# Kernel optimization log

Measured on AMD Instinct MI355X. Metric: run time of the kernel, lower is better.

## Reference

```python
import jax, jax.numpy as jnp
import numpy as np

N = 20000        # nodes (atoms)
E = 256000       # edges
H = 128          # hidden_channels == num_filters
NG = 150         # num_gaussians
L = 3            # num_interactions
B = 16           # graphs in batch
VOCAB = 256      # embed_size
CUTOFF = 15.0
LOG2 = 0.6931471805599453


def _ssp(x):
    # ShiftedSoftplus
    return jax.nn.softplus(x) - LOG2


def setup_inputs() -> dict:
    key = jax.random.key(0)
    ks = jax.random.split(key, 20)

    def w(k, shape, fan_in):
        return jax.random.normal(k, shape, jnp.float32) / np.float32(np.sqrt(fan_in))

    return {
        "z": jax.random.randint(ks[0], (N,), 0, VOCAB),
        "pos": jax.random.normal(ks[1], (N, 3), jnp.float32) * 5.0,
        "batch": jnp.sort(jax.random.randint(ks[2], (N,), 0, B)),
        "edge_index": jax.random.randint(ks[3], (2, E), 0, N),
        # parameters (weights stored as [in, out]; y = x @ W + b)
        "emb": w(ks[4], (VOCAB, H), H),
        "eu0_fc1_w": w(ks[5], (NG + 2 * H, 2 * H), NG + 2 * H),  # EdgeUpdate block 0
        "eu_fc1_w": w(ks[6], (L - 1, 3 * H, 2 * H), 3 * H),      # EdgeUpdate blocks 1..L-1
        "eu_fc1_b": jnp.zeros((L, 2 * H), jnp.float32),
        "eu_fc2_w": w(ks[7], (L, 2 * H, H), 2 * H),
        "eu_fc2_b": jnp.zeros((L, H), jnp.float32),
        "flt_w1": w(ks[8], (L, H, H), H),  # filter_mlp linear 1
        "flt_b1": jnp.zeros((L, H), jnp.float32),
        "flt_w2": w(ks[9], (L, H, H), H),  # filter_mlp linear 2
        "flt_b2": jnp.zeros((L, H), jnp.float32),
        "cf_w": w(ks[10], (L, H, H), H),   # CFConv.fc1 (no bias)
        "st_w1": w(ks[11], (L, H, H), H),  # StateMLP fc1 (no bias)
        "st_w2": w(ks[12], (L, H, H), H),  # StateMLP fc2 (no bias)
        "out_fc1_w": w(ks[13], (H, H // 2), H),
        "out_fc1_b": jnp.zeros((H // 2,), jnp.float32),
        "out_fc2_w": w(ks[14], (H // 2, 1), H // 2),
        "out_fc2_b": jnp.zeros((1,), jnp.float32),
    }


def reference(z, pos, batch, edge_index, emb, eu0_fc1_w, eu_fc1_w, eu_fc1_b,
              eu_fc2_w, eu_fc2_b, flt_w1, flt_b1, flt_w2, flt_b2, cf_w,
              st_w1, st_w2, out_fc1_w, out_fc1_b, out_fc2_w, out_fc2_b):
    row, col = edge_index[0], edge_index[1]  # source j -> target i

    h = emb[z]  # [N, H]

    # Gaussian smearing of interatomic distances
    d = jnp.linalg.norm(pos[row] - pos[col], axis=-1)  # [E]
    stop = CUTOFF - CUTOFF / NG
    offset = jnp.linspace(0.0, stop, NG, dtype=jnp.float32)
    coeff = -0.5 / (stop / (NG - 1)) ** 2
    e = jnp.exp(coeff * (d[:, None] - offset[None, :]) ** 2)  # [E, NG]

    for i in range(L):
        # EdgeUpdate: gather x_i/x_j, concat, 2-layer MLP
        cat = jnp.concatenate([h[col], h[row], e], axis=1)
        w1 = eu0_fc1_w if i == 0 else eu_fc1_w[i - 1]
        e = _ssp(cat @ w1 + eu_fc1_b[i]) @ eu_fc2_w[i] + eu_fc2_b[i]  # [E, H]

        # InteractionBlock: CFConv (filter MLP on edges, gather, modulate, scatter-add)
        W = _ssp(_ssp(e @ flt_w1[i] + flt_b1[i]) @ flt_w2[i] + flt_b2[i])  # [E, H]
        msg = (h[row] @ cf_w[i]) * W                                        # [E, H]
        m = jax.ops.segment_sum(msg, col, num_segments=N)                   # [N, H]
        # StateMLP + residual
        h = h + _ssp(m @ st_w1[i]) @ st_w2[i]

    # readout head
    h = _ssp(h @ out_fc1_w + out_fc1_b) @ out_fc2_w + out_fc2_b  # [N, 1]
    out = jax.ops.segment_sum(h, batch, num_segments=B)          # [B, 1] (readout='add')
    return out
```

## Files before the change

kernel.cpp:

```cpp
#include <hip/hip_runtime.h>
#include <hip/hip_bf16.h>
#include <math.h>

#define NN 20000
#define EE 256000
#define HH 128
#define NGAUSS 150

typedef __attribute__((ext_vector_type(8))) short bf16x8;
typedef __attribute__((ext_vector_type(4))) float f32x4;

__device__ __forceinline__ short f2bf(float f) {
  unsigned u = __builtin_bit_cast(unsigned, f);
  u += 0x7FFFu + ((u >> 16) & 1u);
  return (short)(u >> 16);
}
__device__ __forceinline__ float bf2f(short s) {
  unsigned u = ((unsigned)(unsigned short)s) << 16;
  return __builtin_bit_cast(float, u);
}
__device__ __forceinline__ float sspf(float x) {
  float t = __expf(-fabsf(x));
  return fmaxf(x, 0.f) + __logf(1.f + t) - 0.69314718055994531f;
}

struct PackDesc { const float* src; short* dst; int Kreal; int KT; int NT; int end; };
struct PackArgs { PackDesc d[24]; };

__global__ void packall_kernel(PackArgs a, int total) {
  int idx = blockIdx.x * 256 + threadIdx.x;
  if (idx >= total) return;
  int i = 0, start = 0;
  while (idx >= a.d[i].end) { start = a.d[i].end; ++i; }
  int local = idx - start;
  const float* src = a.d[i].src;
  short* dst = a.d[i].dst;
  int Kreal = a.d[i].Kreal, KT = a.d[i].KT, NT = a.d[i].NT;
  (void)KT;
  int j = local & 7;
  int lane = (local >> 3) & 63;
  int tile = local >> 9;
  int nt = tile % NT, kt = tile / NT;
  int k = kt * 32 + (lane >> 4) * 8 + j;
  int n = nt * 16 + (lane & 15);
  float w = (k < Kreal) ? src[(size_t)k * (NT * 16) + n] : 0.f;
  dst[local] = f2bf(w);
}

template <int KT, int NTW, int JSTEP = 1>
__device__ __forceinline__ void gemm_tile(const short* __restrict__ A, int as,
                                          const short* __restrict__ pack, int ktBase,
                                          int NT, int lane, int wave,
                                          f32x4 (&acc)[NTW][4]) {
  constexpr int WSTEP = (JSTEP == 1) ? NTW : 1;
  const int arow = lane & 15, agrp = lane >> 4;
  const short* abase = A + arow * as + agrp * 8;
  const short* bbase = pack + (size_t)ktBase * NT * 512 + (size_t)lane * 8;
  const int nt0 = wave * WSTEP;
  bf16x8 af[4], bh[NTW];
#pragma unroll
  for (int rg = 0; rg < 4; ++rg) af[rg] = *(const bf16x8*)(abase + rg * 16 * as);
#pragma unroll
  for (int j = 0; j < NTW; ++j)
    bh[j] = *(const bf16x8*)(bbase + (size_t)(nt0 + j * JSTEP) * 512);
#pragma unroll
  for (int kt = 0; kt < KT; ++kt) {
    bf16x8 naf[4], nbh[NTW];
    if (kt + 1 < KT) {
#pragma unroll
      for (int rg = 0; rg < 4; ++rg)
        naf[rg] = *(const bf16x8*)(abase + rg * 16 * as + (kt + 1) * 32);
#pragma unroll
      for (int j = 0; j < NTW; ++j)
        nbh[j] = *(const bf16x8*)(bbase + (size_t)((kt + 1) * NT + nt0 + j * JSTEP) * 512);
    }
#pragma unroll
    for (int j = 0; j < NTW; ++j)
#pragma unroll
      for (int rg = 0; rg < 4; ++rg)
        acc[j][rg] = __builtin_amdgcn_mfma_f32_16x16x32_bf16(af[rg], bh[j], acc[j][rg], 0, 0, 0);
    if (kt + 1 < KT) {
#pragma unroll
      for (int rg = 0; rg < 4; ++rg) af[rg] = naf[rg];
#pragma unroll
      for (int j = 0; j < NTW; ++j) bh[j] = nbh[j];
    }
  }
}

__device__ __forceinline__ void cvt16(const float4* __restrict__ src, short* dst) {
#pragma unroll
  for (int v = 0; v < 2; ++v) {
    float4 f0 = src[2 * v], f1 = src[2 * v + 1];
    union { short s[8]; uint4 u; } tm;
    tm.s[0] = f2bf(f0.x); tm.s[1] = f2bf(f0.y); tm.s[2] = f2bf(f0.z); tm.s[3] = f2bf(f0.w);
    tm.s[4] = f2bf(f1.x); tm.s[5] = f2bf(f1.y); tm.s[6] = f2bf(f1.z); tm.s[7] = f2bf(f1.w);
    *(uint4*)(dst + v * 8) = tm.u;
  }
}

__global__ __launch_bounds__(512, 4) void embedgemm_kernel(
    const int* __restrict__ z, const float* __restrict__ emb,
    const short* __restrict__ pk, short* __restrict__ h, short* __restrict__ hcf) {
  __shared__ short A[64 * 136];
  const int t = threadIdx.x, wave = t >> 6, lane = t & 63;
  const int arow = lane & 15, agrp = lane >> 4;
  const int n0 = blockIdx.x * 64;
  {
    int el = t >> 3, q = t & 7;
    int n = n0 + el;
    short* dst = A + el * 136 + q * 16;
    if (n < NN) {
      const float4* src = (const float4*)(emb + (size_t)z[n] * HH + q * 16);
      union { short s[16]; uint4 u[2]; } tm;
#pragma unroll
      for (int v = 0; v < 2; ++v) {
        float4 f0 = src[2 * v], f1 = src[2 * v + 1];
        tm.s[v * 8 + 0] = f2bf(f0.x); tm.s[v * 8 + 1] = f2bf(f0.y);
        tm.s[v * 8 + 2] = f2bf(f0.z); tm.s[v * 8 + 3] = f2bf(f0.w);
        tm.s[v * 8 + 4] = f2bf(f1.x); tm.s[v * 8 + 5] = f2bf(f1.y);
        tm.s[v * 8 + 6] = f2bf(f1.z); tm.s[v * 8 + 7] = f2bf(f1.w);
      }
      *(uint4*)dst = tm.u[0]; *(uint4*)(dst + 8) = tm.u[1];
      uint4* hg = (uint4*)(h + (size_t)n * HH + q * 16);
      hg[0] = tm.u[0]; hg[1] = tm.u[1];
    } else {
      uint4 zz = {0u, 0u, 0u, 0u};
      *(uint4*)dst = zz; *(uint4*)(dst + 8) = zz;
    }
  }
  __syncthreads();
  f32x4 zv = {0.f, 0.f, 0.f, 0.f};
  f32x4 acc[1][4];
#pragma unroll
  for (int rg = 0; rg < 4; ++rg) acc[0][rg] = zv;
  gemm_tile<4, 1>(A, 136, pk, 0, 8, lane, wave, acc);
  int col = wave * 16 + arow;
#pragma unroll
  for (int rg = 0; rg < 4; ++rg)
#pragma unroll
    for (int r = 0; r < 4; ++r) {
      int n = n0 + rg * 16 + agrp * 4 + r;
      if (n < NN) hcf[(size_t)n * HH + col] = f2bf(acc[0][rg][r]);
    }
}

template <bool FUSE>
__global__ __launch_bounds__(512, 4) void state_kernel(
    short* __restrict__ h, float* __restrict__ m,
    const short* __restrict__ p1, const short* __restrict__ p2,
    const short* __restrict__ pcf, short* __restrict__ hcf) {
  __shared__ short A[64 * 136];
  __shared__ short T[64 * 136];
  const int t = threadIdx.x, wave = t >> 6, lane = t & 63;
  const int arow = lane & 15, agrp = lane >> 4;
  const int n0 = blockIdx.x * 64;
  {
    int el = t >> 3, q = t & 7;
    int n = n0 + el;
    short* dst = A + el * 136 + q * 16;
    if (n < NN) {
      float* msrc = m + (size_t)n * HH + q * 16;
      cvt16((const float4*)msrc, dst);
      if (FUSE) {
        float4 z4 = {0.f, 0.f, 0.f, 0.f};
        float4* mz = (float4*)msrc;
        mz[0] = z4; mz[1] = z4; mz[2] = z4; mz[3] = z4;
      }
    } else {
      uint4 zz = {0u, 0u, 0u, 0u};
      *(uint4*)dst = zz; *(uint4*)(dst + 8) = zz;
    }
  }
  __syncthreads();
  f32x4 zv = {0.f, 0.f, 0.f, 0.f};
  f32x4 acc[1][4];
#pragma unroll
  for (int rg = 0; rg < 4; ++rg) acc[0][rg] = zv;
  gemm_tile<4, 1>(A, 136, p1, 0, 8, lane, wave, acc);
  int col = wave * 16 + arow;
#pragma unroll
  for (int rg = 0; rg < 4; ++rg)
#pragma unroll
    for (int r = 0; r < 4; ++r) {
      int rowl = rg * 16 + agrp * 4 + r;
      T[rowl * 136 + col] = f2bf(sspf(acc[0][rg][r]));
    }
  __syncthreads();
  short hold[16];
#pragma unroll
  for (int rg = 0; rg < 4; ++rg)
#pragma unroll
    for (int r = 0; r < 4; ++r) {
      int n = n0 + rg * 16 + agrp * 4 + r;
      hold[rg * 4 + r] = (n < NN) ? h[(size_t)n * HH + col] : (short)0;
    }
  f32x4 acc2[1][4];
#pragma unroll
  for (int rg = 0; rg < 4; ++rg) acc2[0][rg] = zv;
  gemm_tile<4, 1>(T, 136, p2, 0, 8, lane, wave, acc2);
#pragma unroll
  for (int rg = 0; rg < 4; ++rg)
#pragma unroll
    for (int r = 0; r < 4; ++r) {
      int rowl = rg * 16 + agrp * 4 + r;
      int n = n0 + rowl;
      short nb = f2bf(bf2f(hold[rg * 4 + r]) + acc2[0][rg][r]);
      if (n < NN) h[(size_t)n * HH + col] = nb;
      if (FUSE) A[rowl * 136 + col] = (n < NN) ? nb : (short)0;
    }
  if (FUSE) {
    __syncthreads();
    f32x4 acc3[1][4];
#pragma unroll
    for (int rg = 0; rg < 4; ++rg) acc3[0][rg] = zv;
    gemm_tile<4, 1>(A, 136, pcf, 0, 8, lane, wave, acc3);
#pragma unroll
    for (int rg = 0; rg < 4; ++rg)
#pragma unroll
      for (int r = 0; r < 4; ++r) {
        int n = n0 + rg * 16 + agrp * 4 + r;
        if (n < NN) hcf[(size_t)n * HH + col] = f2bf(acc3[0][rg][r]);
      }
  }
}

template <bool L0, bool WRITE_E>
__global__ __launch_bounds__(512, 4) void edge_kernel(
    const short* __restrict__ h, const short* __restrict__ hcf,
    const int* __restrict__ ei, const float* __restrict__ pos,
    const short* __restrict__ ein, short* __restrict__ eout,
    const short* __restrict__ w1p, const float* __restrict__ b1,
    const short* __restrict__ w2p, const float* __restrict__ b2,
    const short* __restrict__ f1p, const float* __restrict__ fb1,
    const short* __restrict__ f2p, const float* __restrict__ fb2,
    float* __restrict__ m, float gcoeff, float gstep) {
  __shared__ short SBUF[64 * 168];
  __shared__ short ACT[64 * 136];
  __shared__ int RIDX[64], CIDX[64];
  const int t = threadIdx.x;
  const int wave = t >> 6, lane = t & 63;
  const int arow = lane & 15, agrp = lane >> 4;
  const int e0 = blockIdx.x * 64;

  if (t < 64) RIDX[t] = ei[e0 + t];
  else if (t < 128) CIDX[t - 64] = ei[EE + e0 + t - 64];
  __syncthreads();

  const int el = t >> 3, q = t & 7;
  f32x4 zv = {0.f, 0.f, 0.f, 0.f};
  f32x4 acc1[2][4];
#pragma unroll
  for (int j = 0; j < 2; ++j)
#pragma unroll
    for (int rg = 0; rg < 4; ++rg) acc1[j][rg] = zv;

  for (int split = 0; split < 3; ++split) {
    if (split < 2) {
      int node = (split == 0) ? CIDX[el] : RIDX[el];
      const uint4* src = (const uint4*)(h + (size_t)node * HH + q * 16);
      uint4* dst = (uint4*)(SBUF + el * 168 + q * 16);
      dst[0] = src[0]; dst[1] = src[1];
    } else if (L0) {
      int rn = RIDX[el], cn = CIDX[el];
      float dx = pos[rn * 3 + 0] - pos[cn * 3 + 0];
      float dy = pos[rn * 3 + 1] - pos[cn * 3 + 1];
      float dz = pos[rn * 3 + 2] - pos[cn * 3 + 2];
      float d = sqrtf(dx * dx + dy * dy + dz * dz);
#pragma unroll
      for (int i2 = 0; i2 < 20; ++i2) {
        int k = q * 20 + i2;
        float val = 0.f;
        if (k < NGAUSS) { float u = d - (float)k * gstep; val = __expf(gcoeff * u * u); }
        SBUF[el * 168 + k] = f2bf(val);
      }
    } else {
      const uint4* src = (const uint4*)(ein + (size_t)(e0 + el) * HH + q * 16);
      uint4* dst = (uint4*)(SBUF + el * 168 + q * 16);
      dst[0] = src[0]; dst[1] = src[1];
    }
    __syncthreads();
    if (split < 2)
      gemm_tile<4, 2, 8>(SBUF, 168, w1p, split * 4, 16, lane, wave, acc1);
    else if (L0)
      gemm_tile<5, 2, 8>(SBUF, 168, w1p, 8, 16, lane, wave, acc1);
    else
      gemm_tile<4, 2, 8>(SBUF, 168, w1p, 8, 16, lane, wave, acc1);
    __syncthreads();
  }

  const int col = wave * 16 + arow;

  f32x4 acc2[1][4];
#pragma unroll
  for (int rg = 0; rg < 4; ++rg) acc2[0][rg] = zv;
#pragma unroll
  for (int half = 0; half < 2; ++half) {
    float bias = b1[half * 128 + col];
#pragma unroll
    for (int rg = 0; rg < 4; ++rg)
#pragma unroll
      for (int r = 0; r < 4; ++r) {
        int rowl = rg * 16 + agrp * 4 + r;
        ACT[rowl * 136 + col] = f2bf(sspf(acc1[half][rg][r] + bias));
      }
    __syncthreads();
    gemm_tile<4, 1>(ACT, 136, w2p, half * 4, 8, lane, wave, acc2);
    __syncthreads();
  }

  {
    float bias = b2[col];
#pragma unroll
    for (int rg = 0; rg < 4; ++rg)
#pragma unroll
      for (int r = 0; r < 4; ++r) {
        int rowl = rg * 16 + agrp * 4 + r;
        float ev = acc2[0][rg][r] + bias;
        short eb = f2bf(ev);
        if (WRITE_E) eout[(size_t)(e0 + rowl) * HH + col] = eb;
        SBUF[rowl * 136 + col] = eb;
      }
  }
  short hvreg[16];
#pragma unroll
  for (int rg = 0; rg < 4; ++rg)
#pragma unroll
    for (int r = 0; r < 4; ++r) {
      int rowl = rg * 16 + agrp * 4 + r;
      hvreg[rg * 4 + r] = hcf[(size_t)RIDX[rowl] * HH + col];
    }
  __syncthreads();

  f32x4 acc3[1][4];
#pragma unroll
  for (int rg = 0; rg < 4; ++rg) acc3[0][rg] = zv;
  gemm_tile<4, 1>(SBUF, 136, f1p, 0, 8, lane, wave, acc3);
  {
    float bias = fb1[col];
#pragma unroll
    for (int rg = 0; rg < 4; ++rg)
#pragma unroll
      for (int r = 0; r < 4; ++r) {
        int rowl = rg * 16 + agrp * 4 + r;
        ACT[rowl * 136 + col] = f2bf(sspf(acc3[0][rg][r] + bias));
      }
  }
  __syncthreads();

  f32x4 acc4[1][4];
#pragma unroll
  for (int rg = 0; rg < 4; ++rg) acc4[0][rg] = zv;
  gemm_tile<4, 1>(ACT, 136, f2p, 0, 8, lane, wave, acc4);
  {
    float bias = fb2[col];
#pragma unroll
    for (int rg = 0; rg < 4; ++rg)
#pragma unroll
      for (int r = 0; r < 4; ++r) {
        int rowl = rg * 16 + agrp * 4 + r;
        float wv = sspf(acc4[0][rg][r] + bias);
        float hv = bf2f(hvreg[rg * 4 + r]);
        atomicAdd(&m[(size_t)CIDX[rowl] * HH + col], wv * hv);
      }
  }
}

__global__ __launch_bounds__(512, 2) void readout_kernel(
    const short* __restrict__ h, const int* __restrict__ batch,
    const short* __restrict__ pro, const float* __restrict__ b1,
    const float* __restrict__ w2, const float* __restrict__ b2,
    float* __restrict__ out) {
  __shared__ char RAW[128 * 272];
  __shared__ float bacc[16];
  short* A = (short*)RAW;
  float* VAL = (float*)RAW;
  const int t = threadIdx.x, wave = t >> 6, lane = t & 63;
  const int arow = lane & 15, agrp = lane >> 4;
  const int n0 = blockIdx.x * 128;
  if (t < 16) bacc[t] = 0.f;
  {
    int row = t >> 2, qq = t & 3;
    int n = n0 + row;
    uint4* dst = (uint4*)(A + row * 136);
    if (n < NN) {
      const uint4* src = (const uint4*)(h + (size_t)n * HH);
#pragma unroll
      for (int v = 0; v < 4; ++v) dst[qq * 4 + v] = src[qq * 4 + v];
    } else {
      uint4 zz = {0u, 0u, 0u, 0u};
#pragma unroll
      for (int v = 0; v < 4; ++v) dst[qq * 4 + v] = zz;
    }
  }
  __syncthreads();
  f32x4 zv = {0.f, 0.f, 0.f, 0.f};
  f32x4 acc[1][4];
#pragma unroll
  for (int rg = 0; rg < 4; ++rg) acc[0][rg] = zv;
  const short* Abase = A + (wave >> 2) * 64 * 136;
  gemm_tile<4, 1>(Abase, 136, pro, 0, 4, lane, wave & 3, acc);
  __syncthreads();
  {
    int col = (wave & 3) * 16 + arow;
    float bias = b1[col], wv2 = w2[col];
#pragma unroll
    for (int rg = 0; rg < 4; ++rg)
#pragma unroll
      for (int r = 0; r < 4; ++r) {
        int row = (wave >> 2) * 64 + rg * 16 + agrp * 4 + r;
        VAL[row * 68 + col] = sspf(acc[0][rg][r] + bias) * wv2;
      }
  }
  __syncthreads();
  if (t < 128) {
    int n = n0 + t;
    if (n < NN) {
      float s = 0.f;
#pragma unroll 8
      for (int c = 0; c < 64; ++c) s += VAL[t * 68 + c];
      atomicAdd(&bacc[batch[n]], s + b2[0]);
    }
  }
  __syncthreads();
  if (t < 16 && bacc[t] != 0.f) atomicAdd(&out[t], bacc[t]);
}

extern "C" void kernel_launch(void* const* d_in, const int* in_sizes, int n_in,
                              void* d_out, int out_size, void* d_ws, size_t ws_size,
                              hipStream_t stream) {
  const int* z = (const int*)d_in[0];
  const float* pos = (const float*)d_in[1];
  const int* batch = (const int*)d_in[2];
  const int* ei = (const int*)d_in[3];
  const float* emb = (const float*)d_in[4];
  const float* eu0_fc1_w = (const float*)d_in[5];
  const float* eu_fc1_w = (const float*)d_in[6];
  const float* eu_fc1_b = (const float*)d_in[7];
  const float* eu_fc2_w = (const float*)d_in[8];
  const float* eu_fc2_b = (const float*)d_in[9];
  const float* flt_w1 = (const float*)d_in[10];
  const float* flt_b1 = (const float*)d_in[11];
  const float* flt_w2 = (const float*)d_in[12];
  const float* flt_b2 = (const float*)d_in[13];
  const float* cf_w = (const float*)d_in[14];
  const float* st_w1 = (const float*)d_in[15];
  const float* st_w2 = (const float*)d_in[16];
  const float* out_fc1_w = (const float*)d_in[17];
  const float* out_fc1_b = (const float*)d_in[18];
  const float* out_fc2_w = (const float*)d_in[19];
  const float* out_fc2_b = (const float*)d_in[20];
  float* out = (float*)d_out;

  char* p = (char*)d_ws;
  short* h = (short*)p;   p += (size_t)NN * HH * 2;
  short* hcf = (short*)p; p += (size_t)NN * HH * 2;
  float* m = (float*)p;   p += (size_t)NN * HH * 4;
  short* ebuf = (short*)p; p += (size_t)EE * HH * 2;
  auto alloc_pack = [&](int KT, int NT) {
    short* r = (short*)p;
    p += (size_t)KT * NT * 512 * 2;
    return r;
  };
  short* p_eu0 = alloc_pack(13, 16);
  short* p_eu1[2]; for (int l = 0; l < 2; ++l) p_eu1[l] = alloc_pack(12, 16);
  short* p_fc2[3]; for (int l = 0; l < 3; ++l) p_fc2[l] = alloc_pack(8, 8);
  short* p_f1[3], *p_f2[3], *p_cf[3], *p_st1[3], *p_st2[3];
  for (int l = 0; l < 3; ++l) {
    p_f1[l] = alloc_pack(4, 8); p_f2[l] = alloc_pack(4, 8);
    p_cf[l] = alloc_pack(4, 8); p_st1[l] = alloc_pack(4, 8); p_st2[l] = alloc_pack(4, 8);
  }
  short* p_ro = alloc_pack(4, 4);

  PackArgs pa;
  int off = 0, nd = 0;
  auto addpack = [&](const float* src, short* dst, int Kreal, int KT, int NT) {
    off += KT * NT * 512;
    pa.d[nd].src = src; pa.d[nd].dst = dst;
    pa.d[nd].Kreal = Kreal; pa.d[nd].KT = KT; pa.d[nd].NT = NT; pa.d[nd].end = off;
    ++nd;
  };
  addpack(eu0_fc1_w, p_eu0, 406, 13, 16);
  for (int l = 0; l < 2; ++l) addpack(eu_fc1_w + (size_t)l * 384 * 256, p_eu1[l], 384, 12, 16);
  for (int l = 0; l < 3; ++l) addpack(eu_fc2_w + (size_t)l * 256 * 128, p_fc2[l], 256, 8, 8);
  for (int l = 0; l < 3; ++l) {
    addpack(flt_w1 + (size_t)l * 16384, p_f1[l], 128, 4, 8);
    addpack(flt_w2 + (size_t)l * 16384, p_f2[l], 128, 4, 8);
    addpack(cf_w + (size_t)l * 16384, p_cf[l], 128, 4, 8);
    addpack(st_w1 + (size_t)l * 16384, p_st1[l], 128, 4, 8);
    addpack(st_w2 + (size_t)l * 16384, p_st2[l], 128, 4, 8);
  }
  addpack(out_fc1_w, p_ro, 128, 4, 4);
  for (int i = nd; i < 24; ++i) pa.d[i].end = off;
  packall_kernel<<<(off + 255) / 256, 256, 0, stream>>>(pa, off);

  hipMemsetAsync(d_out, 0, 16 * sizeof(float), stream);
  hipMemsetAsync(m, 0, (size_t)NN * HH * 4, stream);
  embedgemm_kernel<<<313, 512, 0, stream>>>(z, emb, p_cf[0], h, hcf);

  double stop = 15.0 - 15.0 / 150.0;
  double step = stop / 149.0;
  float gstep = (float)step;
  float gcoeff = (float)(-0.5 / (step * step));

  for (int i = 0; i < 3; ++i) {
    const short* w1p = (i == 0) ? p_eu0 : p_eu1[i - 1];
    if (i == 0)
      edge_kernel<true, true><<<4000, 512, 0, stream>>>(
          h, hcf, ei, pos, ebuf, ebuf, w1p, eu_fc1_b + (size_t)i * 256,
          p_fc2[i], eu_fc2_b + (size_t)i * 128, p_f1[i], flt_b1 + (size_t)i * 128,
          p_f2[i], flt_b2 + (size_t)i * 128, m, gcoeff, gstep);
    else if (i == 1)
      edge_kernel<false, true><<<4000, 512, 0, stream>>>(
          h, hcf, ei, pos, ebuf, ebuf, w1p, eu_fc1_b + (size_t)i * 256,
          p_fc2[i], eu_fc2_b + (size_t)i * 128, p_f1[i], flt_b1 + (size_t)i * 128,
          p_f2[i], flt_b2 + (size_t)i * 128, m, gcoeff, gstep);
    else
      edge_kernel<false, false><<<4000, 512, 0, stream>>>(
          h, hcf, ei, pos, ebuf, ebuf, w1p, eu_fc1_b + (size_t)i * 256,
          p_fc2[i], eu_fc2_b + (size_t)i * 128, p_f1[i], flt_b1 + (size_t)i * 128,
          p_f2[i], flt_b2 + (size_t)i * 128, m, gcoeff, gstep);
    if (i < 2)
      state_kernel<true><<<313, 512, 0, stream>>>(h, m, p_st1[i], p_st2[i], p_cf[i + 1], hcf);
    else
      state_kernel<false><<<313, 512, 0, stream>>>(h, m, p_st1[i], p_st2[i], nullptr, nullptr);
  }

  readout_kernel<<<157, 512, 0, stream>>>(h, batch, p_ro, out_fc1_b,
                                          out_fc2_w, out_fc2_b, out);
}
```

Before: 604.4 us.

## Add second LDS buffer to overlap edge-feature loads with GEMM and cut barriers

The edge kernel gets an extra shared buffer, so the x_i and x_j node rows are gathered together. The edge-feature or position loads are issued before the second fc1 partial GEMM, so their latency hides behind compute. Both halves of the fc1 activation are written at once, and the two fc2 partial GEMMs run back to back, which removes several __syncthreads. This uses about 17KB more LDS per block, which may lower occupancy under launch_bounds(512,4) and add register pressure.

```diff
diff --git a/kernel.cpp b/kernel.cpp
--- a/kernel.cpp
+++ b/kernel.cpp
@@ -35,8 +35,7 @@
   int local = idx - start;
   const float* src = a.d[i].src;
   short* dst = a.d[i].dst;
-  int Kreal = a.d[i].Kreal, KT = a.d[i].KT, NT = a.d[i].NT;
-  (void)KT;
+  int Kreal = a.d[i].Kreal, NT = a.d[i].NT;
   int j = local & 7;
   int lane = (local >> 3) & 63;
   int tile = local >> 9;
@@ -236,6 +235,7 @@
     const short* __restrict__ f2p, const float* __restrict__ fb2,
     float* __restrict__ m, float gcoeff, float gstep) {
   __shared__ short SBUF[64 * 168];
+  __shared__ short BUF1[64 * 136];
   __shared__ short ACT[64 * 136];
   __shared__ int RIDX[64], CIDX[64];
   const int t = threadIdx.x;
@@ -255,59 +255,70 @@
 #pragma unroll
     for (int rg = 0; rg < 4; ++rg) acc1[j][rg] = zv;
 
-  for (int split = 0; split < 3; ++split) {
-    if (split < 2) {
-      int node = (split == 0) ? CIDX[el] : RIDX[el];
-      const uint4* src = (const uint4*)(h + (size_t)node * HH + q * 16);
-      uint4* dst = (uint4*)(SBUF + el * 168 + q * 16);
-      dst[0] = src[0]; dst[1] = src[1];
-    } else if (L0) {
-      int rn = RIDX[el], cn = CIDX[el];
-      float dx = pos[rn * 3 + 0] - pos[cn * 3 + 0];
-      float dy = pos[rn * 3 + 1] - pos[cn * 3 + 1];
-      float dz = pos[rn * 3 + 2] - pos[cn * 3 + 2];
-      float d = sqrtf(dx * dx + dy * dy + dz * dz);
-#pragma unroll
-      for (int i2 = 0; i2 < 20; ++i2) {
-        int k = q * 20 + i2;
-        float val = 0.f;
-        if (k < NGAUSS) { float u = d - (float)k * gstep; val = __expf(gcoeff * u * u); }
-        SBUF[el * 168 + k] = f2bf(val);
-      }
-    } else {
-      const uint4* src = (const uint4*)(ein + (size_t)(e0 + el) * HH + q * 16);
-      uint4* dst = (uint4*)(SBUF + el * 168 + q * 16);
-      dst[0] = src[0]; dst[1] = src[1];
-    }
-    __syncthreads();
-    if (split < 2)
-      gemm_tile<4, 2, 8>(SBUF, 168, w1p, split * 4, 16, lane, wave, acc1);
-    else if (L0)
-      gemm_tile<5, 2, 8>(SBUF, 168, w1p, 8, 16, lane, wave, acc1);
-    else
-      gemm_tile<4, 2, 8>(SBUF, 168, w1p, 8, 16, lane, wave, acc1);
-    __syncthreads();
-  }
+  {
+    const uint4* csrc = (const uint4*)(h + (size_t)CIDX[el] * HH + q * 16);
+    const uint4* rsrc = (const uint4*)(h + (size_t)RIDX[el] * HH + q * 16);
+    uint4 c0 = csrc[0], c1 = csrc[1];
+    uint4 r0 = rsrc[0], r1 = rsrc[1];
+    uint4* cdst = (uint4*)(SBUF + el * 168 + q * 16);
+    uint4* rdst = (uint4*)(BUF1 + el * 136 + q * 16);
+    cdst[0] = c0; cdst[1] = c1;
+    rdst[0] = r0; rdst[1] = r1;
+  }
+  __syncthreads();
+  gemm_tile<4, 2, 8>(SBUF, 168, w1p, 0, 16, lane, wave, acc1);
+  __syncthreads();
+
+  uint4 eva, evb;
+  float pxr, pyr, pzr, pxc, pyc, pzc;
+  if (L0) {
+    int rn = RIDX[el], cn = CIDX[el];
+    pxr = pos[rn * 3 + 0]; pyr = pos[rn * 3 + 1]; pzr = pos[rn * 3 + 2];
+    pxc = pos[cn * 3 + 0]; pyc = pos[cn * 3 + 1]; pzc = pos[cn * 3 + 2];
+  } else {
+    const uint4* esrc = (const uint4*)(ein + (size_t)(e0 + el) * HH + q * 16);
+    eva = esrc[0]; evb = esrc[1];
+  }
+  gemm_tile<4, 2, 8>(BUF1, 136, w1p, 4, 16, lane, wave, acc1);
+  if (L0) {
+    float dx = pxr - pxc, dy = pyr - pyc, dz = pzr - pzc;
+    float d = sqrtf(dx * dx + dy * dy + dz * dz);
+#pragma unroll
+    for (int i2 = 0; i2 < 20; ++i2) {
+      int k = q * 20 + i2;
+      float val = 0.f;
+      if (k < NGAUSS) { float u = d - (float)k * gstep; val = __expf(gcoeff * u * u); }
+      SBUF[el * 168 + k] = f2bf(val);
+    }
+  } else {
+    uint4* dst = (uint4*)(SBUF + el * 168 + q * 16);
+    dst[0] = eva; dst[1] = evb;
+  }
+  __syncthreads();
+  if (L0)
+    gemm_tile<5, 2, 8>(SBUF, 168, w1p, 8, 16, lane, wave, acc1);
+  else
+    gemm_tile<4, 2, 8>(SBUF, 168, w1p, 8, 16, lane, wave, acc1);
 
   const int col = wave * 16 + arow;
 
-  f32x4 acc2[1][4];
-#pragma unroll
-  for (int rg = 0; rg < 4; ++rg) acc2[0][rg] = zv;
-#pragma unroll
-  for (int half = 0; half < 2; ++half) {
-    float bias = b1[half * 128 + col];
+  {
+    float bias0 = b1[col], bias1 = b1[128 + col];
 #pragma unroll
     for (int rg = 0; rg < 4; ++rg)
 #pragma unroll
       for (int r = 0; r < 4; ++r) {
         int rowl = rg * 16 + agrp * 4 + r;
-        ACT[rowl * 136 + col] = f2bf(sspf(acc1[half][rg][r] + bias));
-      }
-    __syncthreads();
-    gemm_tile<4, 1>(ACT, 136, w2p, half * 4, 8, lane, wave, acc2);
-    __syncthreads();
-  }
+        ACT[rowl * 136 + col] = f2bf(sspf(acc1[0][rg][r] + bias0));
+        BUF1[rowl * 136 + col] = f2bf(sspf(acc1[1][rg][r] + bias1));
+      }
+  }
+  __syncthreads();
+  f32x4 acc2[1][4];
+#pragma unroll
+  for (int rg = 0; rg < 4; ++rg) acc2[0][rg] = zv;
+  gemm_tile<4, 1>(ACT, 136, w2p, 0, 8, lane, wave, acc2);
+  gemm_tile<4, 1>(BUF1, 136, w2p, 4, 8, lane, wave, acc2);
 
   {
     float bias = b2[col];
```

Result: no change. 598.3 us (-1.0%).
